# Kernel optimization log

Hardware: AMD Instinct MI355X
Metric: run time of the kernel (lower is better)

Reference implementation:

```python
import jax, jax.numpy as jnp
import numpy as np

TEMPERATURE = 0.07

def l2norm(x, eps=1e-12):
    # torch.nn.functional.normalize(dim=1): x / max(||x||, eps)
    n = jnp.sqrt(jnp.sum(x * x, axis=1, keepdims=True))
    return x / jnp.maximum(n, eps)

def setup_inputs() -> dict:
    key = jax.random.key(0)
    ks = jax.random.split(key, 8)
    B, D_in, H, M, Q, NNEG = 1024, 2048, 1024, 256, 65536, 16384
    return {
        "y1": jax.random.normal(ks[0], (B, D_in), dtype=jnp.float32),
        "y2": jax.random.normal(ks[1], (B, D_in), dtype=jnp.float32),
        "W_enc_q": jax.random.normal(ks[2], (D_in, H), dtype=jnp.float32) * 0.02,
        "W_enc_k": jax.random.normal(ks[3], (D_in, H), dtype=jnp.float32) * 0.02,
        "W_proj": jax.random.normal(ks[4], (H, M), dtype=jnp.float32) * 0.02,
        "queue": jax.random.normal(ks[5], (Q, M), dtype=jnp.float32),
        "sample_idx": jax.random.randint(ks[6], (NNEG,), 0, Q, dtype=jnp.int32),
        "write_idx": jnp.arange(B, dtype=jnp.int32),
    }

def reference(y1, y2, W_enc_q, W_enc_k, W_proj, queue, sample_idx, write_idx):
    # query path (trainable)
    q = l2norm((y2 @ W_enc_q) @ W_proj)                 # [B, M]
    # key path (no_grad in original)
    k = jax.lax.stop_gradient(l2norm((y1 @ W_enc_k) @ W_proj))  # [B, M]
    # sample negatives from GPU-resident queue (gather) + normalize
    neg = l2norm(queue[sample_idx])                     # [NNEG, M]
    pos_logits = jnp.sum(q * k, axis=1, keepdims=True)  # [B, 1]
    neg_logits = q @ neg.T                              # [B, NNEG]
    logits = jnp.concatenate([pos_logits, neg_logits], axis=1) / TEMPERATURE
    # cross_entropy with labels == 0
    loss = -jnp.mean(jax.nn.log_softmax(logits, axis=-1)[:, 0])
    # FIFO append modeled as circular-buffer scatter write
    new_queue = queue.at[write_idx].set(k)
    return loss, new_queue
```

## Files before the change

### kernel.cpp

```cpp
#include <hip/hip_runtime.h>
#include <hip/hip_bf16.h>
#include <math.h>
#include <stdint.h>


typedef __attribute__((ext_vector_type(4))) float floatx4;
typedef __attribute__((ext_vector_type(8))) short bf16x8;
typedef __attribute__((ext_vector_type(8))) unsigned short ushort8;

__device__ __forceinline__ unsigned short f2bf(float x) {
    union { float f; unsigned int u; } v; v.f = x;
    unsigned int r = v.u + 0x7FFFu + ((v.u >> 16) & 1u);
    return (unsigned short)(r >> 16);
}

__device__ __forceinline__ void async_cp16(const void* g, void* l) {
    auto gp = reinterpret_cast<const __attribute__((address_space(1))) unsigned int*>(
        reinterpret_cast<uintptr_t>(g));
    auto lp = reinterpret_cast<__attribute__((address_space(3))) unsigned int*>(
        reinterpret_cast<uintptr_t>(l));
    __builtin_amdgcn_global_load_lds(gp, lp, 16, 0, 0);
}

__global__ __launch_bounds__(256) void prep_small(
    const float* __restrict__ y2, const float* __restrict__ y1,
    unsigned short* __restrict__ y2b, unsigned short* __restrict__ y1b,
    const float* __restrict__ Wq, const float* __restrict__ Wk,
    const float* __restrict__ Wp,
    unsigned short* __restrict__ Wqt, unsigned short* __restrict__ Wkt,
    unsigned short* __restrict__ Wpt,
    int D, int H, int M) {
    __shared__ unsigned short tile[32][33];
    const int b = blockIdx.x, t = threadIdx.x;
    const int nCastY = 1024;
    const int nTW = (D / 32) * (H / 32);

    if (b < 2 * nCastY) {
        const float* in = (b < nCastY) ? y2 : y1;
        unsigned short* outp = (b < nCastY) ? y2b : y1b;
        long i = (long)(b % nCastY) * 256 + t;
        const float4* in4 = (const float4*)in;
        float4 a = in4[i * 2], c = in4[i * 2 + 1];
        ushort8 o;
        o[0] = f2bf(a.x); o[1] = f2bf(a.y); o[2] = f2bf(a.z); o[3] = f2bf(a.w);
        o[4] = f2bf(c.x); o[5] = f2bf(c.y); o[6] = f2bf(c.z); o[7] = f2bf(c.w);
        ((ushort8*)outp)[i] = o;
        return;
    }
    int bb = b - 2 * nCastY;
    const float* in; unsigned short* outp; int R, C, idx;
    if (bb < nTW)           { in = Wq; outp = Wqt; R = D; C = H; idx = bb; }
    else if (bb < 2 * nTW)  { in = Wk; outp = Wkt; R = D; C = H; idx = bb - nTW; }
    else                    { in = Wp; outp = Wpt; R = H; C = M; idx = bb - 2 * nTW; }
    int cb = C / 32;
    int c0 = (idx % cb) * 32, r0 = (idx / cb) * 32;
    int tx = t & 31, ty = t >> 5;
#pragma unroll
    for (int i = 0; i < 4; ++i)
        tile[ty + i * 8][tx] = f2bf(in[(size_t)(r0 + ty + i * 8) * C + c0 + tx]);
    __syncthreads();
#pragma unroll
    for (int i = 0; i < 4; ++i)
        outp[(size_t)(c0 + ty + i * 8) * R + r0 + tx] = tile[tx][ty + i * 8];
}

__global__ __launch_bounds__(256) void enc_plus(
    const unsigned short* __restrict__ Yb,
    const unsigned short* __restrict__ Wt,
    unsigned short* __restrict__ T12b,
    const float4* __restrict__ queue4, float4* __restrict__ newq4,
    const float* __restrict__ queue, const int* __restrict__ sidx,
    unsigned short* __restrict__ negb) {
    __shared__ unsigned short As[128 * 32];
    __shared__ unsigned short Bs[64 * 32];
    const int b = blockIdx.x, t = threadIdx.x;
    const int type = b % 7, id = b / 7;

    if (type == 0) {
        const int batch = id >> 7, rem = id & 127;
        const int col0 = (rem & 15) * 64, row0 = (rem >> 4) * 128;
        const unsigned short* A = Yb + (long)batch * 1024 * 2048;
        const unsigned short* Bp = Wt + (long)batch * 1024 * 2048;
        unsigned short* C = T12b + (long)batch * 1024 * 1024;
        const int Ko = 2048, No = 1024;
        const int lane = t & 63, wave = t >> 6;
        const int wr = wave >> 1, wc = wave & 1;
        const int lrow = lane & 15, quad = lane >> 4;

        floatx4 acc[4][2] = {};
        for (int kk = 0; kk < Ko; kk += 32) {
            int c0 = t, c1 = t + 256;
            async_cp16(A + (size_t)(row0 + (c0 >> 2)) * Ko + kk + (c0 & 3) * 8,
                       (char*)As + (size_t)c0 * 16);
            async_cp16(A + (size_t)(row0 + (c1 >> 2)) * Ko + kk + (c1 & 3) * 8,
                       (char*)As + (size_t)c1 * 16);
            async_cp16(Bp + (size_t)(col0 + (t >> 2)) * Ko + kk + (t & 3) * 8,
                       (char*)Bs + (size_t)t * 16);
            __syncthreads();
            bf16x8 af[4], bf[2];
#pragma unroll
            for (int i = 0; i < 4; ++i)
                af[i] = *(const bf16x8*)(As + (size_t)(wr * 64 + i * 16 + lrow) * 32 + quad * 8);
#pragma unroll
            for (int j = 0; j < 2; ++j)
                bf[j] = *(const bf16x8*)(Bs + (size_t)(wc * 32 + j * 16 + lrow) * 32 + quad * 8);
#pragma unroll
            for (int i = 0; i < 4; ++i)
#pragma unroll
                for (int j = 0; j < 2; ++j)
                    acc[i][j] = __builtin_amdgcn_mfma_f32_16x16x32_bf16(af[i], bf[j], acc[i][j], 0, 0, 0);
            __syncthreads();
        }
#pragma unroll
        for (int i = 0; i < 4; ++i) {
            int grow = row0 + wr * 64 + i * 16 + quad * 4;
#pragma unroll
            for (int j = 0; j < 2; ++j) {
                int gcol = col0 + wc * 32 + j * 16 + lrow;
#pragma unroll
                for (int r = 0; r < 4; ++r)
                    C[(size_t)(grow + r) * No + gcol] = f2bf(acc[i][j][r]);
            }
        }
    } else if (type == 3 || type == 6) {
        const int gid = id * 2 + (type == 6);
        const int w = t >> 6, lane = t & 63;
#pragma unroll
        for (int j = 0; j < 8; ++j) {
            int r = gid * 32 + w * 8 + j;
            const float4* src = (const float4*)(queue + (size_t)sidx[r] * 256);
            float4 v = src[lane];
            float ss = v.x * v.x + v.y * v.y + v.z * v.z + v.w * v.w;
#pragma unroll
            for (int off = 1; off < 64; off <<= 1) ss += __shfl_xor(ss, off);
            float inv = 1.f / fmaxf(sqrtf(ss), 1e-12f);
            unsigned short o[4] = { f2bf(v.x * inv), f2bf(v.y * inv),
                                    f2bf(v.z * inv), f2bf(v.w * inv) };
            *(unsigned long long*)(negb + (size_t)r * 256 + lane * 4) =
                *(unsigned long long*)o;
        }
    } else {
        const int cid = id * 4 + (type - 1 - (type > 3));
        int base = cid * 4096 + t;
#pragma unroll
        for (int i = 0; i < 16; ++i)
            newq4[base + i * 256] = queue4[base + i * 256];
    }
}

__global__ __launch_bounds__(256) void gemm_proj(const unsigned short* __restrict__ Ag,
                                                 const unsigned short* __restrict__ Bg,
                                                 float* __restrict__ Pg,
                                                 int No, int Ko, int nsplit,
                                                 long sAb) {
    __shared__ unsigned short As[128 * 32];
    __shared__ unsigned short Bs[64 * 32];
    const int z = blockIdx.z;
    const int batch = z / nsplit, split = z - batch * nsplit;
    const unsigned short* A = Ag + (long)batch * sAb;
    const unsigned short* B = Bg;
    float* P = Pg + (long)z * 1024 * No;
    const int Kc = Ko / nsplit, kbeg = split * Kc;
    const int row0 = blockIdx.y * 128, col0 = blockIdx.x * 64;
    const int t = threadIdx.x;
    const int lane = t & 63, wave = t >> 6;
    const int wr = wave >> 1, wc = wave & 1;
    const int lrow = lane & 15, quad = lane >> 4;

    floatx4 acc[4][2] = {};

    for (int kk = kbeg; kk < kbeg + Kc; kk += 32) {
        int c0 = t, c1 = t + 256;
        async_cp16(A + (size_t)(row0 + (c0 >> 2)) * Ko + kk + (c0 & 3) * 8,
                   (char*)As + (size_t)c0 * 16);
        async_cp16(A + (size_t)(row0 + (c1 >> 2)) * Ko + kk + (c1 & 3) * 8,
                   (char*)As + (size_t)c1 * 16);
        async_cp16(B + (size_t)(col0 + (t >> 2)) * Ko + kk + (t & 3) * 8,
                   (char*)Bs + (size_t)t * 16);
        __syncthreads();
        bf16x8 af[4], bf[2];
#pragma unroll
        for (int i = 0; i < 4; ++i)
            af[i] = *(const bf16x8*)(As + (size_t)(wr * 64 + i * 16 + lrow) * 32 + quad * 8);
#pragma unroll
        for (int j = 0; j < 2; ++j)
            bf[j] = *(const bf16x8*)(Bs + (size_t)(wc * 32 + j * 16 + lrow) * 32 + quad * 8);
#pragma unroll
        for (int i = 0; i < 4; ++i)
#pragma unroll
            for (int j = 0; j < 2; ++j)
                acc[i][j] = __builtin_amdgcn_mfma_f32_16x16x32_bf16(af[i], bf[j], acc[i][j], 0, 0, 0);
        __syncthreads();
    }
#pragma unroll
    for (int i = 0; i < 4; ++i) {
        int grow = row0 + wr * 64 + i * 16 + quad * 4;
#pragma unroll
        for (int j = 0; j < 2; ++j) {
            int gcol = col0 + wc * 32 + j * 16 + lrow;
#pragma unroll
            for (int r = 0; r < 4; ++r)
                P[(size_t)(grow + r) * No + gcol] = acc[i][j][r];
        }
    }
}

__global__ __launch_bounds__(256) void qk_finalize(const float* __restrict__ P,
                                                   const int* __restrict__ widx,
                                                   unsigned short* __restrict__ qkb,
                                                   float* __restrict__ newq,
                                                   float* __restrict__ pos,
                                                   float* __restrict__ sumexp,
                                                   int B_, int nsplit, float invT) {
    const int i = blockIdx.x, t = threadIdx.x;
    const long RM = (long)B_ * 256;
    float sq = 0.f, sk = 0.f;
    for (int s = 0; s < nsplit; ++s) {
        sq += P[(long)s * RM + (long)i * 256 + t];
        sk += P[(long)(nsplit + s) * RM + (long)i * 256 + t];
    }
    __shared__ float r0[256], r1[256], r2[256];
    r0[t] = sq * sq; r1[t] = sk * sk; r2[t] = sq * sk;
    __syncthreads();
    for (int off = 128; off > 0; off >>= 1) {
        if (t < off) { r0[t] += r0[t + off]; r1[t] += r1[t + off]; r2[t] += r2[t + off]; }
        __syncthreads();
    }
    float nq = fmaxf(sqrtf(r0[0]), 1e-12f);
    float nk = fmaxf(sqrtf(r1[0]), 1e-12f);
    float qn = sq / nq, kn = sk / nk;
    qkb[(size_t)i * 256 + t] = f2bf(qn);
    qkb[(size_t)(B_ + i) * 256 + t] = f2bf(kn);
    newq[(size_t)widx[i] * 256 + t] = kn;
    if (t == 0) {
        float p = (r2[0] / (nq * nk)) * invT;
        pos[i] = p;
        sumexp[i] = __expf(p);
    }
}

__global__ __launch_bounds__(256) void gemm_logits(const unsigned short* __restrict__ A,
                                                   const unsigned short* __restrict__ B,
                                                   float* __restrict__ sumexp,
                                                   int Ko, float invT) {
    __shared__ unsigned short As[128 * 64];
    __shared__ unsigned short Bs[128 * 64];
    __shared__ float rowred[128];
    const int row0 = blockIdx.y * 128, col0 = blockIdx.x * 128;
    const int t = threadIdx.x;
    const int lane = t & 63, wave = t >> 6;
    const int wr = wave >> 1, wc = wave & 1;
    const int lrow = lane & 15, quad = lane >> 4;

    floatx4 acc[4][4] = {};

    for (int kk = 0; kk < Ko; kk += 64) {
#pragma unroll
        for (int r = 0; r < 4; ++r) {
            int c = t + r * 256;
            async_cp16(A + (size_t)(row0 + (c >> 3)) * Ko + kk + (c & 7) * 8,
                       (char*)As + (size_t)c * 16);
            async_cp16(B + (size_t)(col0 + (c >> 3)) * Ko + kk + (c & 7) * 8,
                       (char*)Bs + (size_t)c * 16);
        }
        __syncthreads();
        bf16x8 af[4][2], bf[4][2];
#pragma unroll
        for (int i = 0; i < 4; ++i)
#pragma unroll
            for (int k2 = 0; k2 < 2; ++k2) {
                af[i][k2] = *(const bf16x8*)(As + (size_t)(wr * 64 + i * 16 + lrow) * 64 + k2 * 32 + quad * 8);
                bf[i][k2] = *(const bf16x8*)(Bs + (size_t)(wc * 64 + i * 16 + lrow) * 64 + k2 * 32 + quad * 8);
            }
#pragma unroll
        for (int k2 = 0; k2 < 2; ++k2)
#pragma unroll
            for (int i = 0; i < 4; ++i)
#pragma unroll
                for (int j = 0; j < 4; ++j)
                    acc[i][j] = __builtin_amdgcn_mfma_f32_16x16x32_bf16(af[i][k2], bf[j][k2], acc[i][j], 0, 0, 0);
        __syncthreads();
    }
    if (t < 128) rowred[t] = 0.f;
    __syncthreads();
#pragma unroll
    for (int i = 0; i < 4; ++i) {
#pragma unroll
        for (int r = 0; r < 4; ++r) {
            float s = 0.f;
#pragma unroll
            for (int j = 0; j < 4; ++j) s += __expf(acc[i][j][r] * invT);
            s += __shfl_xor(s, 1); s += __shfl_xor(s, 2);
            s += __shfl_xor(s, 4); s += __shfl_xor(s, 8);
            if (lrow == 0) atomicAdd(&rowred[wr * 64 + i * 16 + quad * 4 + r], s);
        }
    }
    __syncthreads();
    if (t < 128) atomicAdd(&sumexp[row0 + t], rowred[t]);
}

__global__ __launch_bounds__(256) void final_loss(const float* __restrict__ pos,
                                                  const float* __restrict__ sumexp,
                                                  float* __restrict__ out, int B_) {
    const int t = threadIdx.x;
    float acc = 0.f;
    for (int i = t; i < B_; i += 256) acc += logf(sumexp[i]) - pos[i];
    __shared__ float s[256];
    s[t] = acc;
    __syncthreads();
    for (int off = 128; off > 0; off >>= 1) {
        if (t < off) s[t] += s[t + off];
        __syncthreads();
    }
    if (t == 0) out[0] = s[0] / (float)B_;
}

extern "C" void kernel_launch(void* const* d_in, const int* in_sizes, int n_in,
                              void* d_out, int out_size, void* d_ws, size_t ws_size,
                              hipStream_t stream) {
    const float* y1    = (const float*)d_in[0];
    const float* y2    = (const float*)d_in[1];
    const float* Wq    = (const float*)d_in[2];
    const float* Wk    = (const float*)d_in[3];
    const float* Wp    = (const float*)d_in[4];
    const float* queue = (const float*)d_in[5];
    const int*   sidx  = (const int*)d_in[6];
    const int*   widx  = (const int*)d_in[7];
    float* out = (float*)d_out;

    const int B    = in_sizes[7];
    const int NNEG = in_sizes[6];
    const int D    = in_sizes[0] / B;
    const int H    = in_sizes[2] / D;
    const int M    = in_sizes[4] / H;
    const int Q    = in_sizes[5] / M;
    const float invT = 1.0f / 0.07f;
    const int NS_P = 4;

    float* ws  = (float*)d_ws;
    float* Pp     = ws;
    float* pos    = Pp + (size_t)2 * NS_P * B * M;
    float* sumexp = pos + B;
    unsigned short* us = (unsigned short*)(sumexp + B);
    unsigned short* y2b  = us;
    unsigned short* y1b  = y2b + (size_t)B * D;
    unsigned short* Wqt  = y1b + (size_t)B * D;
    unsigned short* Wkt  = Wqt + (size_t)H * D;
    unsigned short* Wpt  = Wkt + (size_t)H * D;
    unsigned short* T12b = Wpt + (size_t)M * H;
    unsigned short* qkb  = T12b + (size_t)2 * B * H;
    unsigned short* negb = qkb + (size_t)2 * B * M;

    const int nPrep = 2 * 1024 + 2 * (D / 32) * (H / 32) + (H / 32) * (M / 32);
    prep_small<<<nPrep, 256, 0, stream>>>(y2, y1, y2b, y1b, Wq, Wk, Wp,
                                          Wqt, Wkt, Wpt, D, H, M);

    enc_plus<<<1792, 256, 0, stream>>>(y2b, Wqt, T12b,
                                       (const float4*)queue, (float4*)(out + 1),
                                       queue, sidx, negb);

    gemm_proj<<<dim3(M / 64, B / 128, 2 * NS_P), 256, 0, stream>>>(
        T12b, Wpt, Pp, M, H, NS_P, (long)B * H);

    qk_finalize<<<B, 256, 0, stream>>>(Pp, widx, qkb, out + 1, pos, sumexp,
                                       B, NS_P, invT);

    gemm_logits<<<dim3(NNEG / 128, B / 128), 256, 0, stream>>>(
        qkb, negb, sumexp, M, invT);

    final_loss<<<1, 256, 0, stream>>>(pos, sumexp, out, B);
}
```

Baseline: 234.3 us.

## Double-buffer LDS in encoder and projection GEMMs; widen queue-copy blocks

```diff
diff --git a/kernel.cpp b/kernel.cpp
--- a/kernel.cpp
+++ b/kernel.cpp
@@ -71,10 +71,10 @@
     const float4* __restrict__ queue4, float4* __restrict__ newq4,
     const float* __restrict__ queue, const int* __restrict__ sidx,
     unsigned short* __restrict__ negb) {
-    __shared__ unsigned short As[128 * 32];
-    __shared__ unsigned short Bs[64 * 32];
+    __shared__ unsigned short As[2][128 * 32];
+    __shared__ unsigned short Bs[2][64 * 32];
     const int b = blockIdx.x, t = threadIdx.x;
-    const int type = b % 7, id = b / 7;
+    const int type = b % 5, id = b / 5;
 
     if (type == 0) {
         const int batch = id >> 7, rem = id & 127;
@@ -86,31 +86,49 @@
         const int lane = t & 63, wave = t >> 6;
         const int wr = wave >> 1, wc = wave & 1;
         const int lrow = lane & 15, quad = lane >> 4;
+        const int nK = Ko / 32;
 
         floatx4 acc[4][2] = {};
-        for (int kk = 0; kk < Ko; kk += 32) {
+
+        auto stage = [&](int kk, int p) {
             int c0 = t, c1 = t + 256;
             async_cp16(A + (size_t)(row0 + (c0 >> 2)) * Ko + kk + (c0 & 3) * 8,
-                       (char*)As + (size_t)c0 * 16);
+                       (char*)(As[p]) + (size_t)c0 * 16);
             async_cp16(A + (size_t)(row0 + (c1 >> 2)) * Ko + kk + (c1 & 3) * 8,
-                       (char*)As + (size_t)c1 * 16);
+                       (char*)(As[p]) + (size_t)c1 * 16);
             async_cp16(Bp + (size_t)(col0 + (t >> 2)) * Ko + kk + (t & 3) * 8,
-                       (char*)Bs + (size_t)t * 16);
-            __syncthreads();
-            bf16x8 af[4], bf[2];
+                       (char*)(Bs[p]) + (size_t)t * 16);
+        };
+        auto compute = [&](int p) {
+            bf16x8 af[4], bfr[2];
 #pragma unroll
             for (int i = 0; i < 4; ++i)
-                af[i] = *(const bf16x8*)(As + (size_t)(wr * 64 + i * 16 + lrow) * 32 + quad * 8);
+                af[i] = *(const bf16x8*)(As[p] + (size_t)(wr * 64 + i * 16 + lrow) * 32 + quad * 8);
 #pragma unroll
             for (int j = 0; j < 2; ++j)
-                bf[j] = *(const bf16x8*)(Bs + (size_t)(wc * 32 + j * 16 + lrow) * 32 + quad * 8);
+                bfr[j] = *(const bf16x8*)(Bs[p] + (size_t)(wc * 32 + j * 16 + lrow) * 32 + quad * 8);
+            __builtin_amdgcn_s_setprio(1);
 #pragma unroll
             for (int i = 0; i < 4; ++i)
 #pragma unroll
                 for (int j = 0; j < 2; ++j)
-                    acc[i][j] = __builtin_amdgcn_mfma_f32_16x16x32_bf16(af[i], bf[j], acc[i][j], 0, 0, 0);
-            __syncthreads();
-        }
+                    acc[i][j] = __builtin_amdgcn_mfma_f32_16x16x32_bf16(af[i], bfr[j], acc[i][j], 0, 0, 0);
+            __builtin_amdgcn_s_setprio(0);
+        };
+
+        stage(0, 0);
+#pragma unroll 2
+        for (int k = 0; k < nK - 1; ++k) {
+            stage((k + 1) * 32, (k & 1) ^ 1);
+            asm volatile("s_waitcnt vmcnt(3)" ::: "memory");
+            __builtin_amdgcn_s_barrier();
+            compute(k & 1);
+            __builtin_amdgcn_s_barrier();
+        }
+        asm volatile("s_waitcnt vmcnt(0)" ::: "memory");
+        __builtin_amdgcn_s_barrier();
+        compute((nK - 1) & 1);
+
 #pragma unroll
         for (int i = 0; i < 4; ++i) {
             int grow = row0 + wr * 64 + i * 16 + quad * 4;
@@ -122,8 +140,8 @@
                     C[(size_t)(grow + r) * No + gcol] = f2bf(acc[i][j][r]);
             }
         }
-    } else if (type == 3 || type == 6) {
-        const int gid = id * 2 + (type == 6);
+    } else if (type == 2 || type == 4) {
+        const int gid = id * 2 + (type == 4);
         const int w = t >> 6, lane = t & 63;
 #pragma unroll
         for (int j = 0; j < 8; ++j) {
@@ -140,11 +158,16 @@
                 *(unsigned long long*)o;
         }
     } else {
-        const int cid = id * 4 + (type - 1 - (type > 3));
-        int base = cid * 4096 + t;
-#pragma unroll
-        for (int i = 0; i < 16; ++i)
-            newq4[base + i * 256] = queue4[base + i * 256];
+        const int cid = id * 2 + (type == 3);
+        long base = (long)cid * 8192 + t;
+#pragma unroll
+        for (int o = 0; o < 4; ++o) {
+            float4 v[8];
+#pragma unroll
+            for (int i = 0; i < 8; ++i) v[i] = queue4[base + (size_t)(o * 8 + i) * 256];
+#pragma unroll
+            for (int i = 0; i < 8; ++i) newq4[base + (size_t)(o * 8 + i) * 256] = v[i];
+        }
     }
 }
 
@@ -153,8 +176,8 @@
                                                  float* __restrict__ Pg,
                                                  int No, int Ko, int nsplit,
                                                  long sAb) {
-    __shared__ unsigned short As[128 * 32];
-    __shared__ unsigned short Bs[64 * 32];
+    __shared__ unsigned short As[2][128 * 32];
+    __shared__ unsigned short Bs[2][64 * 32];
     const int z = blockIdx.z;
     const int batch = z / nsplit, split = z - batch * nsplit;
     const unsigned short* A = Ag + (long)batch * sAb;
@@ -166,32 +189,48 @@
     const int lane = t & 63, wave = t >> 6;
     const int wr = wave >> 1, wc = wave & 1;
     const int lrow = lane & 15, quad = lane >> 4;
+    const int nIt = Kc / 32;
 
     floatx4 acc[4][2] = {};
 
-    for (int kk = kbeg; kk < kbeg + Kc; kk += 32) {
+    auto stage = [&](int kk, int p) {
         int c0 = t, c1 = t + 256;
         async_cp16(A + (size_t)(row0 + (c0 >> 2)) * Ko + kk + (c0 & 3) * 8,
-                   (char*)As + (size_t)c0 * 16);
+                   (char*)(As[p]) + (size_t)c0 * 16);
         async_cp16(A + (size_t)(row0 + (c1 >> 2)) * Ko + kk + (c1 & 3) * 8,
-                   (char*)As + (size_t)c1 * 16);
+                   (char*)(As[p]) + (size_t)c1 * 16);
         async_cp16(B + (size_t)(col0 + (t >> 2)) * Ko + kk + (t & 3) * 8,
-                   (char*)Bs + (size_t)t * 16);
-        __syncthreads();
-        bf16x8 af[4], bf[2];
+                   (char*)(Bs[p]) + (size_t)t * 16);
+    };
+    auto compute = [&](int p) {
+        bf16x8 af[4], bfr[2];
 #pragma unroll
         for (int i = 0; i < 4; ++i)
-            af[i] = *(const bf16x8*)(As + (size_t)(wr * 64 + i * 16 + lrow) * 32 + quad * 8);
+            af[i] = *(const bf16x8*)(As[p] + (size_t)(wr * 64 + i * 16 + lrow) * 32 + quad * 8);
 #pragma unroll
         for (int j = 0; j < 2; ++j)
-            bf[j] = *(const bf16x8*)(Bs + (size_t)(wc * 32 + j * 16 + lrow) * 32 + quad * 8);
+            bfr[j] = *(const bf16x8*)(Bs[p] + (size_t)(wc * 32 + j * 16 + lrow) * 32 + quad * 8);
+        __builtin_amdgcn_s_setprio(1);
 #pragma unroll
         for (int i = 0; i < 4; ++i)
 #pragma unroll
             for (int j = 0; j < 2; ++j)
-                acc[i][j] = __builtin_amdgcn_mfma_f32_16x16x32_bf16(af[i], bf[j], acc[i][j], 0, 0, 0);
-        __syncthreads();
-    }
+                acc[i][j] = __builtin_amdgcn_mfma_f32_16x16x32_bf16(af[i], bfr[j], acc[i][j], 0, 0, 0);
+        __builtin_amdgcn_s_setprio(0);
+    };
+
+    stage(kbeg, 0);
+    for (int k = 0; k < nIt - 1; ++k) {
+        stage(kbeg + (k + 1) * 32, (k & 1) ^ 1);
+        asm volatile("s_waitcnt vmcnt(3)" ::: "memory");
+        __builtin_amdgcn_s_barrier();
+        compute(k & 1);
+        __builtin_amdgcn_s_barrier();
+    }
+    asm volatile("s_waitcnt vmcnt(0)" ::: "memory");
+    __builtin_amdgcn_s_barrier();
+    compute((nIt - 1) & 1);
+
 #pragma unroll
     for (int i = 0; i < 4; ++i) {
         int grow = row0 + wr * 64 + i * 16 + quad * 4;
@@ -355,7 +394,7 @@
     prep_small<<<nPrep, 256, 0, stream>>>(y2, y1, y2b, y1b, Wq, Wk, Wp,
                                           Wqt, Wkt, Wpt, D, H, M);
 
-    enc_plus<<<1792, 256, 0, stream>>>(y2b, Wqt, T12b,
+    enc_plus<<<1280, 256, 0, stream>>>(y2b, Wqt, T12b,
                                        (const float4*)queue, (float4*)(out + 1),
                                        queue, sidx, negb);
 
```

New measurement: 228.7 us. -2.4%, faster.
